# Performance work log

Hardware: AMD Instinct MI355X
Metric: run time of the kernel (lower is better)

Reference implementation:

```python
import jax, jax.numpy as jnp
import numpy as np

N, B, NPG, E = 16384, 64, 256, 524288
F_IN, POS_DIM, L_PE = 32, 3, 8
W, HEADS, LAYERS, DFF = 256, 8, 2, 1024
HID, OUT = 512, 64
S = NPG + 1
DH = W // HEADS


def _ln(x, s, b, eps=1e-5):
    m = jnp.mean(x, -1, keepdims=True)
    v = jnp.var(x, -1, keepdims=True)
    return (x - m) * jax.lax.rsqrt(v + eps) * s + b


def _gelu(x):
    # custom tanh-approx GELU from the source module
    c = float(np.sqrt(2.0 / np.pi))
    return 0.5 * x * (1.0 + jnp.tanh(c * (x + 0.044715 * x ** 3)))


def setup_inputs() -> dict:
    key = jax.random.key(0)
    ks = jax.random.split(key, 24)
    nrm = lambda k, shape, s=0.05: jax.random.normal(k, shape, jnp.float32) * s
    D_IN = F_IN + POS_DIM * L_PE  # 56
    inp = {}
    inp['x'] = jax.random.normal(ks[0], (N, F_IN), jnp.float32)
    inp['p'] = jax.random.uniform(ks[1], (N, POS_DIM), jnp.float32, -1.0, 1.0)
    inp['edge_index'] = jax.random.randint(ks[2], (2, E), 0, N, jnp.int32)
    inp['batch'] = (jnp.arange(N) // NPG).astype(jnp.int32)  # sorted, 64 equal graphs
    inp['gcn_w'] = nrm(ks[3], (D_IN, W), 0.1)
    inp['gcn_b'] = jnp.zeros((W,), jnp.float32)
    inp['cls_token'] = nrm(ks[4], (1, 1, W), 0.02)
    inp['ln_pre_s'] = jnp.ones((W,), jnp.float32)
    inp['ln_pre_b'] = jnp.zeros((W,), jnp.float32)
    inp['norm1_s'] = jnp.ones((LAYERS, W), jnp.float32)
    inp['norm1_b'] = jnp.zeros((LAYERS, W), jnp.float32)
    inp['in_proj_w'] = nrm(ks[5], (LAYERS, W, 3 * W))
    inp['in_proj_b'] = jnp.zeros((LAYERS, 3 * W), jnp.float32)
    inp['out_proj_w'] = nrm(ks[6], (LAYERS, W, W))
    inp['out_proj_b'] = jnp.zeros((LAYERS, W), jnp.float32)
    inp['norm2_s'] = jnp.ones((LAYERS, W), jnp.float32)
    inp['norm2_b'] = jnp.zeros((LAYERS, W), jnp.float32)
    inp['ff_w1'] = nrm(ks[7], (LAYERS, W, DFF))
    inp['ff_b1'] = jnp.zeros((LAYERS, DFF), jnp.float32)
    inp['ff_w2'] = nrm(ks[8], (LAYERS, DFF, W))
    inp['ff_b2'] = jnp.zeros((LAYERS, W), jnp.float32)
    inp['ln_post_s'] = jnp.ones((W,), jnp.float32)
    inp['ln_post_b'] = jnp.zeros((W,), jnp.float32)
    inp['dec_w1'] = nrm(ks[9], (W, HID))
    inp['dec_b1'] = jnp.zeros((HID,), jnp.float32)
    inp['dec_w2'] = nrm(ks[10], (HID, HID))
    inp['dec_b2'] = jnp.zeros((HID,), jnp.float32)
    inp['dec_w3'] = nrm(ks[11], (HID, OUT))
    inp['dec_b3'] = jnp.zeros((OUT,), jnp.float32)
    return inp


def _forward(x, p, gcn_w, gcn_b, cls_token, ln_pre_s, ln_pre_b, norm1_s, norm1_b,
             in_proj_w, in_proj_b, out_proj_w, out_proj_b, norm2_s, norm2_b,
             ff_w1, ff_b1, ff_w2, ff_b2, ln_post_s, ln_post_b,
             dec_w1, dec_b1, dec_w2, dec_b2, dec_w3, dec_b3, edge_index, batch):
    # positional encoding: sin(p * 2^i * pi), i = 0..L-1
    freqs = (2.0 ** jnp.arange(L_PE, dtype=jnp.float32)) * jnp.pi
    pe = jnp.sin(p[:, :, None] * freqs).reshape(N, POS_DIM * L_PE)
    xc = jnp.concatenate([x, pe], axis=-1)  # [N, 56]
    # GCNConv: x W, then sym-normalized aggregation with self loops, + bias
    xw = xc @ gcn_w  # [N, W]
    loop = jnp.arange(N, dtype=edge_index.dtype)
    row = jnp.concatenate([edge_index[0], loop])
    col = jnp.concatenate([edge_index[1], loop])
    deg = jax.ops.segment_sum(jnp.ones_like(row, dtype=xw.dtype), col, num_segments=N)
    dinv = jax.lax.rsqrt(jnp.maximum(deg, 1e-12))
    coef = dinv[row] * dinv[col]
    h = jax.ops.segment_sum(coef[:, None] * xw[row], col, num_segments=N) + gcn_b
    # to_dense_batch (batch is sorted graph ids)
    counts = jax.ops.segment_sum(jnp.ones((N,), jnp.int32), batch, num_segments=B)
    ptr = jnp.concatenate([jnp.zeros((1,), jnp.int32), jnp.cumsum(counts)[:-1]])
    pos = jnp.arange(N, dtype=jnp.int32) - ptr[batch]
    dense = jnp.zeros((B, NPG, W), h.dtype).at[batch, pos].set(h)
    mask = jnp.zeros((B, NPG), bool).at[batch, pos].set(True)
    # prepend cls token
    xd = jnp.concatenate([jnp.broadcast_to(cls_token, (B, 1, W)), dense], axis=1)  # [B,S,W]
    valid = jnp.concatenate([jnp.ones((B, 1), bool), mask], axis=1)  # [B,S]
    xd = _ln(xd, ln_pre_s, ln_pre_b)
    # causal mask with row 0 (cls) unmasked
    am = jnp.triu(jnp.ones((S, S), bool), k=1)
    am = am.at[0, :].set(False)
    allowed = (~am)[None, :, :] & valid[:, None, :]  # [B,S,S]
    scale = 1.0 / float(np.sqrt(DH))
    for l in range(LAYERS):
        h1 = _ln(xd, norm1_s[l], norm1_b[l])
        qkv = h1 @ in_proj_w[l] + in_proj_b[l]  # [B,S,3W]
        q, k, v = jnp.split(qkv, 3, axis=-1)
        q = q.reshape(B, S, HEADS, DH)
        k = k.reshape(B, S, HEADS, DH)
        v = v.reshape(B, S, HEADS, DH)
        sc = jnp.einsum('bqhd,bkhd->bhqk', q, k) * scale
        sc = jnp.where(allowed[:, None, :, :], sc, -1e9)
        a = jax.nn.softmax(sc, axis=-1)
        o = jnp.einsum('bhqk,bkhd->bqhd', a, v).reshape(B, S, W)
        xd = xd + (o @ out_proj_w[l] + out_proj_b[l])
        h2 = _ln(xd, norm2_s[l], norm2_b[l])
        # MLP(num_layers=2) applies activation after BOTH layers (incl. last)
        ff = _gelu(_gelu(h2 @ ff_w1[l] + ff_b1[l]) @ ff_w2[l] + ff_b2[l])
        xd = xd + ff
    cls = _ln(xd[:, 0, :], ln_post_s, ln_post_b)
    # decoder MLP(num_layers=3) with relu after every layer (incl. last)
    h3 = jax.nn.relu(cls @ dec_w1 + dec_b1)
    h3 = jax.nn.relu(h3 @ dec_w2 + dec_b2)
    return jax.nn.relu(h3 @ dec_w3 + dec_b3)


def reference(x, p, gcn_w, gcn_b, cls_token, ln_pre_s, ln_pre_b, norm1_s, norm1_b,
              in_proj_w, in_proj_b, out_proj_w, out_proj_b, norm2_s, norm2_b,
              ff_w1, ff_b1, ff_w2, ff_b2, ln_post_s, ln_post_b,
              dec_w1, dec_b1, dec_w2, dec_b2, dec_w3, dec_b3, edge_index, batch):
    return _forward(x, p, gcn_w, gcn_b, cls_token, ln_pre_s, ln_pre_b, norm1_s, norm1_b,
                    in_proj_w, in_proj_b, out_proj_w, out_proj_b, norm2_s, norm2_b,
                    ff_w1, ff_b1, ff_w2, ff_b2, ln_post_s, ln_post_b,
                    dec_w1, dec_b1, dec_w2, dec_b2, dec_w3, dec_b3, edge_index, batch)
```

## Files before the change

kernel.cpp:

```cpp
#include <hip/hip_runtime.h>
#include <math.h>

constexpr int N_NODES = 16384;
constexpr int BGRAPH  = 64;
constexpr int NEDGE   = 524288;
constexpr int SEQ     = 257;
constexpr int WDIM    = 256;
constexpr int DFF     = 1024;
constexpr int HID     = 512;
constexpr int MROWS   = BGRAPH * SEQ;

constexpr size_t F_Y    = 0;
constexpr size_t F_AGG  = F_Y    + (size_t)N_NODES * 64;
constexpr size_t F_XD   = F_AGG  + (size_t)N_NODES * 64;
constexpr size_t F_CLS  = F_XD   + (size_t)MROWS * WDIM;
constexpr size_t F_D1   = F_CLS  + (size_t)BGRAPH * WDIM;
constexpr size_t F_D2   = F_D1   + (size_t)BGRAPH * HID;
constexpr size_t F_WPAD = F_D2   + (size_t)BGRAPH * HID;
constexpr size_t F_DINV = F_WPAD + (size_t)64 * WDIM;
constexpr size_t F_IEND = F_DINV + (size_t)N_NODES;

typedef __attribute__((ext_vector_type(8))) __bf16 bf16x8;
typedef __attribute__((ext_vector_type(4))) __bf16 bf16x4;
typedef __attribute__((ext_vector_type(4))) float f32x4;

__device__ __forceinline__ float gelu_f(float x) {
    float u = 0.7978845608028654f * (x + 0.044715f * x * x * x);
    return 0.5f * x * (1.0f + tanhf(u));
}

__global__ __launch_bounds__(256) void hist_kernel(const int* __restrict__ col, int* __restrict__ indeg) {
    int e = blockIdx.x * 256 + threadIdx.x;
    atomicAdd(&indeg[col[e]], 1);
}

__global__ __launch_bounds__(1024) void scan_kernel(const int* __restrict__ indeg, int* __restrict__ offs,
                                                    int* __restrict__ cursor, float* __restrict__ dinv) {
    __shared__ int parts[1024];
    int t = threadIdx.x;
    int base = t * 16;
    int loc[16];
    int s = 0;
#pragma unroll
    for (int i = 0; i < 16; ++i) { loc[i] = indeg[base + i]; s += loc[i]; }
    parts[t] = s;
    __syncthreads();
    for (int off = 1; off < 1024; off <<= 1) {
        int v = (t >= off) ? parts[t - off] : 0;
        __syncthreads();
        parts[t] += v;
        __syncthreads();
    }
    int run = (t == 0) ? 0 : parts[t - 1];
#pragma unroll
    for (int i = 0; i < 16; ++i) {
        offs[base + i] = run;
        cursor[base + i] = run;
        dinv[base + i] = rsqrtf((float)loc[i] + 1.0f);
        run += loc[i];
    }
    if (t == 1023) offs[N_NODES] = run;
}

__global__ __launch_bounds__(256) void fill_kernel(const int* __restrict__ ei, int* __restrict__ cursor,
                                                   int* __restrict__ csr) {
    int e = blockIdx.x * 256 + threadIdx.x;
    int r = ei[e];
    int c = ei[NEDGE + e];
    int pos = atomicAdd(&cursor[c], 1);
    csr[pos] = r;
}

__global__ __launch_bounds__(256) void y_kernel(const float* __restrict__ x, const float* __restrict__ p,
                                                const float* __restrict__ dinv, float* __restrict__ y) {
    int idx = blockIdx.x * 256 + threadIdx.x;
    int i = idx >> 6, d = idx & 63;
    float v = 0.f;
    if (d < 32) {
        v = x[i * 32 + d];
    } else if (d < 56) {
        int dd = d - 32;
        int dim = dd >> 3, j = dd & 7;
        v = sinf(p[i * 3 + dim] * (3.14159265358979323846f * (float)(1 << j)));
    }
    y[idx] = dinv[i] * v;
}

__global__ __launch_bounds__(256) void agg_kernel(const float* __restrict__ y, const float* __restrict__ dinv,
                                                  const int* __restrict__ offs, const int* __restrict__ csr,
                                                  float* __restrict__ agg) {
    int c = (blockIdx.x * 256 + threadIdx.x) >> 6;
    int lane = threadIdx.x & 63;
    float acc = y[(size_t)c * 64 + lane];
    int s = offs[c], e = offs[c + 1];
    for (int j = s; j < e; ++j) {
        int r = csr[j];
        acc += y[(size_t)r * 64 + lane];
    }
    agg[(size_t)c * 64 + lane] = dinv[c] * acc;
}

__global__ __launch_bounds__(256) void wpad_kernel(const float* __restrict__ w, float* __restrict__ wp) {
    int idx = blockIdx.x * 256 + threadIdx.x;
    wp[idx] = (idx < 56 * 256) ? w[idx] : 0.f;
}

__global__ __launch_bounds__(256) void cls_write(const float* __restrict__ tok, float* __restrict__ xd) {
    xd[(size_t)blockIdx.x * SEQ * WDIM + threadIdx.x] = tok[threadIdx.x];
}

template <int OUTBF>
__global__ __launch_bounds__(256) void ln4_kernel(const float* __restrict__ in, int rin_stride,
                                                  void* __restrict__ out,
                                                  const float* __restrict__ g, const float* __restrict__ be) {
    int w = threadIdx.x >> 6, lane = threadIdx.x & 63;
    int row = blockIdx.x * 4 + w;
    const float* ip = in + (size_t)row * rin_stride + lane * 4;
    f32x4 v = *(const f32x4*)ip;
    float s = v[0] + v[1] + v[2] + v[3];
    float ss = v[0] * v[0] + v[1] * v[1] + v[2] * v[2] + v[3] * v[3];
#pragma unroll
    for (int off = 1; off < 64; off <<= 1) { s += __shfl_xor(s, off); ss += __shfl_xor(ss, off); }
    float mean = s * 0.00390625f;
    float var = ss * 0.00390625f - mean * mean;
    float rs = rsqrtf(var + 1e-5f);
    f32x4 gv = *(const f32x4*)(g + lane * 4);
    f32x4 bv = *(const f32x4*)(be + lane * 4);
    if (OUTBF) {
        bf16x4 o;
#pragma unroll
        for (int i = 0; i < 4; ++i) o[i] = (__bf16)((v[i] - mean) * rs * gv[i] + bv[i]);
        *(bf16x4*)((__bf16*)out + (size_t)row * 256 + lane * 4) = o;
    } else {
        f32x4 o;
#pragma unroll
        for (int i = 0; i < 4; ++i) o[i] = (v[i] - mean) * rs * gv[i] + bv[i];
        *(f32x4*)((float*)out + (size_t)row * 256 + lane * 4) = o;
    }
}

__global__ __launch_bounds__(256) void tcast_kernel(const float* __restrict__ W, __bf16* __restrict__ Wt,
                                                    int K, int N) {
    __shared__ __bf16 T[64][65];
    int t = threadIdx.x;
    int k0 = blockIdx.x << 6, n0 = blockIdx.y << 6;
#pragma unroll
    for (int i = 0; i < 16; ++i) {
        int idx = t + i * 256;
        int k = idx >> 6, n = idx & 63;
        T[k][n] = (__bf16)W[(size_t)(k0 + k) * N + n0 + n];
    }
    __syncthreads();
#pragma unroll
    for (int i = 0; i < 16; ++i) {
        int idx = t + i * 256;
        int n = idx >> 6, k = idx & 63;
        Wt[(size_t)(n0 + n) * K + k0 + k] = T[k][n];
    }
}

constexpr int LP = 36;
template <int BN, int ACT, int OMODE>
__global__ __launch_bounds__(256) void gemm_bf(const __bf16* __restrict__ A, int lda,
                                               const __bf16* __restrict__ Bt,
                                               const float* __restrict__ bias,
                                               void* __restrict__ Cv, int ldc,
                                               int Ktot, int Mrows, int MBlocks, int NY) {
    constexpr int NTW = BN / 32;
    constexpr int AH = 128 * LP;
    constexpr int BH = BN * LP;
    __shared__ __bf16 As[2 * 128 * LP];
    __shared__ __bf16 Bs[2 * BN * LP];
    int f = blockIdx.x;
    int m8 = f & 7;
    int rest = f >> 3;
    int mg = rest / NY;
    int yb = rest - mg * NY;
    int mb = mg * 8 + m8;
    if (mb >= MBlocks) return;
    int m0 = mb << 7, n0 = yb * BN;

    int t = threadIdx.x;
    int w = t >> 6, L = t & 63;
    int wm = w >> 1, wn = w & 1;
    int lc = L & 15, quad = L >> 4;

    int sa_row = t >> 1, sa_off = (t & 1) << 4;
    const __bf16* ap = A + (size_t)(m0 + sa_row) * lda + sa_off;
    __bf16* as_dst = &As[sa_row * LP + sa_off];
    const __bf16* bp;
    __bf16* bs_dst;
    if constexpr (BN == 128) {
        bp = Bt + (size_t)(n0 + sa_row) * Ktot + sa_off;
        bs_dst = &Bs[sa_row * LP + sa_off];
    } else {
        int sb_row = t >> 2, sb_off = (t & 3) << 3;
        bp = Bt + (size_t)(n0 + sb_row) * Ktot + sb_off;
        bs_dst = &Bs[sb_row * LP + sb_off];
    }

    int a_base = (wm * 64 + lc) * LP + quad * 8;
    int b_base = (wn * (BN / 2) + lc) * LP + quad * 8;

    f32x4 acc[4][NTW] = {};

    bf16x8 ea0, ea1, eb0, eb1, oa0, oa1, ob0, ob1;
    ea0 = *(const bf16x8*)(ap);        ea1 = *(const bf16x8*)(ap + 8);
    oa0 = *(const bf16x8*)(ap + 32);   oa1 = *(const bf16x8*)(ap + 40);
    if constexpr (BN == 128) {
        eb0 = *(const bf16x8*)(bp);        eb1 = *(const bf16x8*)(bp + 8);
        ob0 = *(const bf16x8*)(bp + 32);   ob1 = *(const bf16x8*)(bp + 40);
    } else {
        eb0 = *(const bf16x8*)(bp);
        ob0 = *(const bf16x8*)(bp + 32);
    }

    for (int k0 = 0; k0 < Ktot; k0 += 64) {
        __syncthreads();
        *(bf16x8*)as_dst = ea0;
        *(bf16x8*)(as_dst + 8) = ea1;
        *(bf16x8*)(as_dst + AH) = oa0;
        *(bf16x8*)(as_dst + AH + 8) = oa1;
        if constexpr (BN == 128) {
            *(bf16x8*)bs_dst = eb0;
            *(bf16x8*)(bs_dst + 8) = eb1;
            *(bf16x8*)(bs_dst + BH) = ob0;
            *(bf16x8*)(bs_dst + BH + 8) = ob1;
        } else {
            *(bf16x8*)bs_dst = eb0;
            *(bf16x8*)(bs_dst + BH) = ob0;
        }
        __syncthreads();
        if (k0 + 64 < Ktot) {
            ea0 = *(const bf16x8*)(ap + k0 + 64);
            ea1 = *(const bf16x8*)(ap + k0 + 72);
            oa0 = *(const bf16x8*)(ap + k0 + 96);
            oa1 = *(const bf16x8*)(ap + k0 + 104);
            if constexpr (BN == 128) {
                eb0 = *(const bf16x8*)(bp + k0 + 64);
                eb1 = *(const bf16x8*)(bp + k0 + 72);
                ob0 = *(const bf16x8*)(bp + k0 + 96);
                ob1 = *(const bf16x8*)(bp + k0 + 104);
            } else {
                eb0 = *(const bf16x8*)(bp + k0 + 64);
                ob0 = *(const bf16x8*)(bp + k0 + 96);
            }
        }
        {
            bf16x8 af[4], bfr[NTW];
#pragma unroll
            for (int i = 0; i < 4; ++i) af[i] = *(const bf16x8*)&As[a_base + i * 16 * LP];
#pragma unroll
            for (int i = 0; i < NTW; ++i) bfr[i] = *(const bf16x8*)&Bs[b_base + i * 16 * LP];
#pragma unroll
            for (int mt = 0; mt < 4; ++mt)
#pragma unroll
                for (int nt = 0; nt < NTW; ++nt)
                    acc[mt][nt] = __builtin_amdgcn_mfma_f32_16x16x32_bf16(af[mt], bfr[nt], acc[mt][nt], 0, 0, 0);
        }
        {
            bf16x8 af[4], bfr[NTW];
#pragma unroll
            for (int i = 0; i < 4; ++i) af[i] = *(const bf16x8*)&As[AH + a_base + i * 16 * LP];
#pragma unroll
            for (int i = 0; i < NTW; ++i) bfr[i] = *(const bf16x8*)&Bs[BH + b_base + i * 16 * LP];
#pragma unroll
            for (int mt = 0; mt < 4; ++mt)
#pragma unroll
                for (int nt = 0; nt < NTW; ++nt)
                    acc[mt][nt] = __builtin_amdgcn_mfma_f32_16x16x32_bf16(af[mt], bfr[nt], acc[mt][nt], 0, 0, 0);
        }
    }

#pragma unroll
    for (int mt = 0; mt < 4; ++mt) {
        int gmb = m0 + wm * 64 + mt * 16 + quad * 4;
#pragma unroll
        for (int nt = 0; nt < NTW; ++nt) {
            int gn = n0 + wn * (BN / 2) + nt * 16 + lc;
            float bv = bias[gn];
#pragma unroll
            for (int r = 0; r < 4; ++r) {
                int gm = gmb + r;
                if (gm >= Mrows) continue;
                float v = acc[mt][nt][r] + bv;
                if (ACT == 1) v = gelu_f(v);
                if (OMODE == 0) {
                    ((__bf16*)Cv)[(size_t)gm * ldc + gn] = (__bf16)v;
                } else {
                    float* cp = (float*)Cv + (size_t)gm * ldc + gn;
                    *cp = v + *cp;
                }
            }
        }
    }
}

constexpr int PPITCH = 284;
__global__ __launch_bounds__(256, 2) void attn_mfma(const __bf16* __restrict__ qkvb,
                                                    __bf16* __restrict__ obuf) {
    __shared__ __bf16 Vt[32][PPITCH];
    __shared__ __bf16 Pb[4][16][PPITCH];
    int bb = blockIdx.x;
    int b = bb >> 3, h = bb & 7;
    int t = threadIdx.x;
    int w = t >> 6, L = t & 63;
    int c = L & 15, quad = L >> 4;
    const float scale = 0.17677669529663687f;
    const __bf16* qb = qkvb + (size_t)(b * SEQ) * 768 + h * 32;
    const __bf16* kb = qb + 256;
    const __bf16* vb = qb + 512;
    __bf16* ob = obuf + (size_t)(b * SEQ) * 256 + h * 32;

    for (int idx = t; idx < 272 * 4; idx += 256) {
        int key = idx >> 2, dc = (idx & 3) * 8;
        bf16x8 vv = {};
        if (key < SEQ) vv = *(const bf16x8*)(vb + (size_t)key * 768 + dc);
#pragma unroll
        for (int j = 0; j < 8; ++j) Vt[dc + j][key] = vv[j];
    }

    bf16x8 kfr[17];
#pragma unroll
    for (int tt = 0; tt < 17; ++tt) {
        int kr = tt * 16 + c; if (kr > 256) kr = 256;
        kfr[tt] = *(const bf16x8*)(kb + (size_t)kr * 768 + quad * 8);
    }
    __syncthreads();

#pragma unroll 1
    for (int qt = 0; qt < 5; ++qt) {
        int q0 = qt * 64 + w * 16;
        if (q0 > 256) continue;
        int ntiles = (qt == 0 && w == 0) ? 17 : (qt * 4 + w + 1);
        if (ntiles > 17) ntiles = 17;
        int nkc = (ntiles + 1) >> 1;

        bf16x8 qf;
        {
            int qr = q0 + c; if (qr > 256) qr = 256;
            qf = *(const bf16x8*)(qb + (size_t)qr * 768 + quad * 8);
        }

        f32x4 acc[17];
#pragma unroll
        for (int tt = 0; tt < 17; ++tt) {
            if (tt >= ntiles) continue;
            f32x4 z = {0.f, 0.f, 0.f, 0.f};
            acc[tt] = __builtin_amdgcn_mfma_f32_16x16x32_bf16(qf, kfr[tt], z, 0, 0, 0);
        }

        float inv[4];
#pragma unroll
        for (int j = 0; j < 4; ++j) {
            int q = q0 + quad * 4 + j;
            float mx = -3.0e38f;
#pragma unroll
            for (int tt = 0; tt < 17; ++tt) {
                if (tt >= ntiles) continue;
                int key = tt * 16 + c;
                bool ok = (key < SEQ) && (q == 0 || key <= q);
                float v = ok ? acc[tt][j] * scale : -3.0e38f;
                mx = fmaxf(mx, v);
            }
            mx = fmaxf(mx, __shfl_xor(mx, 1));
            mx = fmaxf(mx, __shfl_xor(mx, 2));
            mx = fmaxf(mx, __shfl_xor(mx, 4));
            mx = fmaxf(mx, __shfl_xor(mx, 8));
            float s = 0.f;
#pragma unroll
            for (int tt = 0; tt < 17; ++tt) {
                if (tt >= ntiles) continue;
                int key = tt * 16 + c;
                bool ok = (key < SEQ) && (q == 0 || key <= q);
                float pv = ok ? expf(acc[tt][j] * scale - mx) : 0.f;
                s += pv;
                Pb[w][quad * 4 + j][key] = (__bf16)pv;
            }
            if ((ntiles & 1) && ntiles < 17)
                Pb[w][quad * 4 + j][ntiles * 16 + c] = (__bf16)0.f;
            s += __shfl_xor(s, 1);
            s += __shfl_xor(s, 2);
            s += __shfl_xor(s, 4);
            s += __shfl_xor(s, 8);
            inv[j] = 1.0f / s;
        }

        f32x4 oacc0 = {0.f, 0.f, 0.f, 0.f};
        f32x4 oacc1 = {0.f, 0.f, 0.f, 0.f};
#pragma unroll
        for (int kc = 0; kc < 9; ++kc) {
            if (kc >= nkc) continue;
            int off = kc * 32 + quad * 8;
            bf16x8 af = {};
            bf16x8 bf0 = {};
            bf16x8 bf1 = {};
            if (off < 257) {
                af  = *(const bf16x8*)&Pb[w][c][off];
                bf0 = *(const bf16x8*)&Vt[c][off];
                bf1 = *(const bf16x8*)&Vt[16 + c][off];
            }
            oacc0 = __builtin_amdgcn_mfma_f32_16x16x32_bf16(af, bf0, oacc0, 0, 0, 0);
            oacc1 = __builtin_amdgcn_mfma_f32_16x16x32_bf16(af, bf1, oacc1, 0, 0, 0);
        }

#pragma unroll
        for (int j = 0; j < 4; ++j) {
            int q = q0 + quad * 4 + j;
            if (q < SEQ) {
                __bf16* op = ob + (size_t)q * 256;
                op[c]      = (__bf16)(oacc0[j] * inv[j]);
                op[16 + c] = (__bf16)(oacc1[j] * inv[j]);
            }
        }
    }
}

template <int ACT, bool RESID, bool REMAP>
__global__ __launch_bounds__(256) void gemm_std(const float* __restrict__ A, int lda,
                                                const float* __restrict__ Bw, int ldb,
                                                const float* __restrict__ bias,
                                                float* __restrict__ C, int ldc, int Ktot) {
    int t = threadIdx.x;
    int m0 = blockIdx.x << 6, n0 = blockIdx.y << 6;
    __shared__ float As[16][68];
    __shared__ float Bs[16][64];
    int arow = t >> 2, akk = (t & 3) << 2;
    int bk = t >> 4, bn = (t & 15) << 2;
    int tm = (t >> 4) << 2, tn = (t & 15) << 2;
    float acc[4][4] = {};
    const float* ap = A + (size_t)(m0 + arow) * lda + akk;
    const float* bp = Bw + (size_t)bk * ldb + n0 + bn;
    for (int k0 = 0; k0 < Ktot; k0 += 16) {
        float4 av = *(const float4*)(ap + k0);
        float4 bv = *(const float4*)(bp + (size_t)k0 * ldb);
        __syncthreads();
        As[akk + 0][arow] = av.x; As[akk + 1][arow] = av.y;
        As[akk + 2][arow] = av.z; As[akk + 3][arow] = av.w;
        *(float4*)&Bs[bk][bn] = bv;
        __syncthreads();
#pragma unroll
        for (int k = 0; k < 16; ++k) {
            float4 a = *(const float4*)&As[k][tm];
            float4 b = *(const float4*)&Bs[k][tn];
            acc[0][0] += a.x * b.x; acc[0][1] += a.x * b.y; acc[0][2] += a.x * b.z; acc[0][3] += a.x * b.w;
            acc[1][0] += a.y * b.x; acc[1][1] += a.y * b.y; acc[1][2] += a.y * b.z; acc[1][3] += a.y * b.w;
            acc[2][0] += a.z * b.x; acc[2][1] += a.z * b.y; acc[2][2] += a.z * b.z; acc[2][3] += a.z * b.w;
            acc[3][0] += a.w * b.x; acc[3][1] += a.w * b.y; acc[3][2] += a.w * b.z; acc[3][3] += a.w * b.w;
        }
    }
#pragma unroll
    for (int i = 0; i < 4; ++i) {
        int gm = m0 + tm + i;
        int orow = REMAP ? (gm + (gm >> 8) + 1) : gm;
        float* cp = C + (size_t)orow * ldc + n0 + tn;
        float4 r;
        r.x = acc[i][0] + bias[n0 + tn + 0];
        r.y = acc[i][1] + bias[n0 + tn + 1];
        r.z = acc[i][2] + bias[n0 + tn + 2];
        r.w = acc[i][3] + bias[n0 + tn + 3];
        if (ACT == 1) { r.x = gelu_f(r.x); r.y = gelu_f(r.y); r.z = gelu_f(r.z); r.w = gelu_f(r.w); }
        if (ACT == 2) { r.x = fmaxf(r.x, 0.f); r.y = fmaxf(r.y, 0.f); r.z = fmaxf(r.z, 0.f); r.w = fmaxf(r.w, 0.f); }
        if (RESID) {
            float4 o = *(const float4*)cp;
            r.x += o.x; r.y += o.y; r.z += o.z; r.w += o.w;
        }
        *(float4*)cp = r;
    }
}

template <int K, int NOUT>
__global__ __launch_bounds__(256) void dec_fc2(const float* __restrict__ in, const float* __restrict__ w,
                                               const float* __restrict__ bia, float* __restrict__ out) {
    __shared__ float rowbuf[K];
    __shared__ float part[4][64];
    int b = blockIdx.x, c = blockIdx.y, t = threadIdx.x;
    for (int i = t; i < K; i += 256) rowbuf[i] = in[(size_t)b * K + i];
    __syncthreads();
    int lane = t & 63, wv = t >> 6;
    int n = c * 64 + lane;
    const int KQ = K / 4;
    const float* wp = w + (size_t)(wv * KQ) * NOUT + n;
    float s = 0.f;
#pragma unroll 8
    for (int k = 0; k < KQ; ++k) s += rowbuf[wv * KQ + k] * wp[(size_t)k * NOUT];
    part[wv][lane] = s;
    __syncthreads();
    if (wv == 0) {
        float r = part[0][lane] + part[1][lane] + part[2][lane] + part[3][lane] + bia[n];
        out[(size_t)b * NOUT + n] = fmaxf(r, 0.f);
    }
}

extern "C" void kernel_launch(void* const* d_in, const int* in_sizes, int n_in,
                              void* d_out, int out_size, void* d_ws, size_t ws_size,
                              hipStream_t stream) {
    const float* x         = (const float*)d_in[0];
    const float* p         = (const float*)d_in[1];
    const int*   ei        = (const int*)d_in[2];
    const float* gcn_w     = (const float*)d_in[4];
    const float* gcn_b     = (const float*)d_in[5];
    const float* cls_tok   = (const float*)d_in[6];
    const float* ln_pre_s  = (const float*)d_in[7];
    const float* ln_pre_b  = (const float*)d_in[8];
    const float* norm1_s   = (const float*)d_in[9];
    const float* norm1_b   = (const float*)d_in[10];
    const float* in_proj_w = (const float*)d_in[11];
    const float* in_proj_b = (const float*)d_in[12];
    const float* out_proj_w= (const float*)d_in[13];
    const float* out_proj_b= (const float*)d_in[14];
    const float* norm2_s   = (const float*)d_in[15];
    const float* norm2_b   = (const float*)d_in[16];
    const float* ff_w1     = (const float*)d_in[17];
    const float* ff_b1     = (const float*)d_in[18];
    const float* ff_w2     = (const float*)d_in[19];
    const float* ff_b2     = (const float*)d_in[20];
    const float* ln_post_s = (const float*)d_in[21];
    const float* ln_post_b = (const float*)d_in[22];
    const float* dec_w1    = (const float*)d_in[23];
    const float* dec_b1    = (const float*)d_in[24];
    const float* dec_w2    = (const float*)d_in[25];
    const float* dec_b2    = (const float*)d_in[26];
    const float* dec_w3    = (const float*)d_in[27];
    const float* dec_b3    = (const float*)d_in[28];

    float* ws   = (float*)d_ws;
    float* y    = ws + F_Y;
    float* agg  = ws + F_AGG;
    float* xd   = ws + F_XD;
    float* cls  = ws + F_CLS;
    float* dd1  = ws + F_D1;
    float* dd2  = ws + F_D2;
    float* wpad = ws + F_WPAD;
    float* dinv = ws + F_DINV;
    int* ibase  = (int*)(ws + F_IEND);
    int* indeg  = ibase;
    int* offs   = ibase + N_NODES;
    int* cursor = offs + N_NODES + 1;
    int* csr    = cursor + N_NODES;
    uintptr_t ub = ((uintptr_t)(csr + NEDGE) + 15) & ~(uintptr_t)15;
    __bf16* h1b  = (__bf16*)ub;
    __bf16* qkvb = h1b  + (size_t)MROWS * 256;
    __bf16* ffbb = qkvb + (size_t)MROWS * 768;
    __bf16* wt_in  = ffbb  + (size_t)MROWS * 1024;
    __bf16* wt_out = wt_in  + 2 * 768 * 256;
    __bf16* wt_f1  = wt_out + 2 * 256 * 256;
    __bf16* wt_f2  = wt_f1  + 2 * 1024 * 256;

    hipMemsetAsync(indeg, 0, N_NODES * sizeof(int), stream);
    hist_kernel<<<NEDGE / 256, 256, 0, stream>>>(ei + NEDGE, indeg);
    scan_kernel<<<1, 1024, 0, stream>>>(indeg, offs, cursor, dinv);
    fill_kernel<<<NEDGE / 256, 256, 0, stream>>>(ei, cursor, csr);
    y_kernel<<<N_NODES * 64 / 256, 256, 0, stream>>>(x, p, dinv, y);
    agg_kernel<<<N_NODES / 4, 256, 0, stream>>>(y, dinv, offs, csr, agg);
    wpad_kernel<<<64, 256, 0, stream>>>(gcn_w, wpad);

    for (int l = 0; l < 2; ++l) {
        tcast_kernel<<<dim3(4, 12), 256, 0, stream>>>(in_proj_w + (size_t)l * 256 * 768,
                                                      wt_in + (size_t)l * 768 * 256, 256, 768);
        tcast_kernel<<<dim3(4, 4), 256, 0, stream>>>(out_proj_w + (size_t)l * 256 * 256,
                                                     wt_out + (size_t)l * 256 * 256, 256, 256);
        tcast_kernel<<<dim3(4, 16), 256, 0, stream>>>(ff_w1 + (size_t)l * 256 * 1024,
                                                      wt_f1 + (size_t)l * 1024 * 256, 256, 1024);
        tcast_kernel<<<dim3(16, 4), 256, 0, stream>>>(ff_w2 + (size_t)l * 1024 * 256,
                                                      wt_f2 + (size_t)l * 256 * 1024, 1024, 256);
    }

    gemm_std<0, false, true><<<dim3(256, 4), 256, 0, stream>>>(agg, 64, wpad, 256, gcn_b, xd, 256, 64);
    cls_write<<<64, 256, 0, stream>>>(cls_tok, xd);
    ln4_kernel<0><<<MROWS / 4, 256, 0, stream>>>(xd, 256, xd, ln_pre_s, ln_pre_b);

    const int MB = (MROWS + 127) / 128;
    const int MG8 = (MB + 7) / 8;
    for (int l = 0; l < 2; ++l) {
        ln4_kernel<1><<<MROWS / 4, 256, 0, stream>>>(xd, 256, h1b, norm1_s + l * WDIM, norm1_b + l * WDIM);
        gemm_bf<128, 0, 0><<<8 * 6 * MG8, 256, 0, stream>>>(
            h1b, 256, wt_in + (size_t)l * 768 * 256, in_proj_b + l * 768, qkvb, 768, 256, MROWS, MB, 6);
        attn_mfma<<<512, 256, 0, stream>>>(qkvb, h1b);
        gemm_bf<64, 0, 1><<<8 * 4 * MG8, 256, 0, stream>>>(
            h1b, 256, wt_out + (size_t)l * 256 * 256, out_proj_b + l * WDIM, xd, 256, 256, MROWS, MB, 4);
        ln4_kernel<1><<<MROWS / 4, 256, 0, stream>>>(xd, 256, h1b, norm2_s + l * WDIM, norm2_b + l * WDIM);
        gemm_bf<128, 1, 0><<<8 * 8 * MG8, 256, 0, stream>>>(
            h1b, 256, wt_f1 + (size_t)l * 1024 * 256, ff_b1 + l * DFF, ffbb, 1024, 256, MROWS, MB, 8);
        gemm_bf<64, 1, 1><<<8 * 4 * MG8, 256, 0, stream>>>(
            ffbb, 1024, wt_f2 + (size_t)l * 256 * 1024, ff_b2 + l * WDIM, xd, 256, 1024, MROWS, MB, 4);
    }

    ln4_kernel<0><<<BGRAPH / 4, 256, 0, stream>>>(xd, SEQ * WDIM, cls, ln_post_s, ln_post_b);
    dec_fc2<256, 512><<<dim3(BGRAPH, 8), 256, 0, stream>>>(cls, dec_w1, dec_b1, dd1);
    dec_fc2<512, 512><<<dim3(BGRAPH, 8), 256, 0, stream>>>(dd1, dec_w2, dec_b2, dd2);
    dec_fc2<512, 64><<<dim3(BGRAPH, 1), 256, 0, stream>>>(dd2, dec_w3, dec_b3, (float*)d_out);
}
```

Before: 714.4 us.

## Compute only the CLS row in the last transformer layer

Only the CLS token of the final layer feeds the output, so the last layer now computes K and V projections for all rows and runs everything else on the CLS row alone. That covers the Q projection, attention, out-projection, LN2 and the FFN, each done in small dedicated kernels over 64 rows. This removes most of the last layer's GEMM and attention work and skips transposing the unused layer-2 weights. The new per-row kernels are simple scalar fp32 loops and may be slow relative to their tiny work, and they mix fp32 and bf16 precision differently than the main path.

```diff
diff --git a/kernel.cpp b/kernel.cpp
--- a/kernel.cpp
+++ b/kernel.cpp
@@ -18,7 +18,8 @@
 constexpr size_t F_D2   = F_D1   + (size_t)BGRAPH * HID;
 constexpr size_t F_WPAD = F_D2   + (size_t)BGRAPH * HID;
 constexpr size_t F_DINV = F_WPAD + (size_t)64 * WDIM;
-constexpr size_t F_IEND = F_DINV + (size_t)N_NODES;
+constexpr size_t F_XCLS = F_DINV + (size_t)N_NODES;
+constexpr size_t F_IEND = F_XCLS + (size_t)BGRAPH * WDIM;
 
 typedef __attribute__((ext_vector_type(8))) __bf16 bf16x8;
 typedef __attribute__((ext_vector_type(4))) __bf16 bf16x4;
@@ -414,6 +415,127 @@
             }
         }
     }
+}
+
+__global__ __launch_bounds__(256) void qcls_kernel(const __bf16* __restrict__ h1b,
+                                                   const float* __restrict__ W,
+                                                   const float* __restrict__ bias,
+                                                   __bf16* __restrict__ qcls) {
+    __shared__ float hrow[256];
+    int b = blockIdx.x, t = threadIdx.x;
+    hrow[t] = (float)h1b[(size_t)(b * SEQ) * 256 + t];
+    __syncthreads();
+    float s = bias[t];
+    for (int k = 0; k < 256; ++k) s += hrow[k] * W[(size_t)k * 768 + t];
+    qcls[b * 256 + t] = (__bf16)s;
+}
+
+__global__ __launch_bounds__(64) void attn_cls(const __bf16* __restrict__ qcls,
+                                               const __bf16* __restrict__ qkvb,
+                                               __bf16* __restrict__ ocls) {
+    __shared__ float p[260];
+    int bb = blockIdx.x;
+    int b = bb >> 3, h = bb & 7;
+    int lane = threadIdx.x;
+    const float scale = 0.17677669529663687f;
+    float q[32];
+    const __bf16* qp = qcls + b * 256 + h * 32;
+#pragma unroll
+    for (int c = 0; c < 4; ++c) {
+        bf16x8 v = *(const bf16x8*)(qp + c * 8);
+#pragma unroll
+        for (int e = 0; e < 8; ++e) q[c * 8 + e] = (float)v[e];
+    }
+    float sc[5];
+    float mx = -3.0e38f;
+#pragma unroll
+    for (int i = 0; i < 5; ++i) {
+        int j = lane + i * 64;
+        float s = -3.0e38f;
+        if (j < SEQ) {
+            const __bf16* kp = qkvb + (size_t)(b * SEQ + j) * 768 + 256 + h * 32;
+            float a = 0.f;
+#pragma unroll
+            for (int c = 0; c < 4; ++c) {
+                bf16x8 v = *(const bf16x8*)(kp + c * 8);
+#pragma unroll
+                for (int e = 0; e < 8; ++e) a += q[c * 8 + e] * (float)v[e];
+            }
+            s = a * scale;
+        }
+        sc[i] = s;
+        mx = fmaxf(mx, s);
+    }
+#pragma unroll
+    for (int off = 1; off < 64; off <<= 1) mx = fmaxf(mx, __shfl_xor(mx, off));
+    float sum = 0.f;
+#pragma unroll
+    for (int i = 0; i < 5; ++i) {
+        int j = lane + i * 64;
+        float e = (j < SEQ) ? expf(sc[i] - mx) : 0.f;
+        sc[i] = e;
+        sum += e;
+    }
+#pragma unroll
+    for (int off = 1; off < 64; off <<= 1) sum += __shfl_xor(sum, off);
+    float inv = 1.0f / sum;
+#pragma unroll
+    for (int i = 0; i < 5; ++i) {
+        int j = lane + i * 64;
+        if (j < SEQ) p[j] = sc[i] * inv;
+    }
+    __syncthreads();
+    if (lane < 32) {
+        float o = 0.f;
+        for (int j = 0; j < SEQ; ++j)
+            o += p[j] * (float)qkvb[(size_t)(b * SEQ + j) * 768 + 512 + h * 32 + lane];
+        ocls[b * 256 + h * 32 + lane] = (__bf16)o;
+    }
+}
+
+__global__ __launch_bounds__(256) void oproj_cls(const __bf16* __restrict__ ocls,
+                                                 const float* __restrict__ W,
+                                                 const float* __restrict__ bias,
+                                                 const float* __restrict__ xd,
+                                                 float* __restrict__ xcls) {
+    __shared__ float orow[256];
+    int b = blockIdx.x, t = threadIdx.x;
+    orow[t] = (float)ocls[b * 256 + t];
+    __syncthreads();
+    float s = bias[t];
+    for (int k = 0; k < 256; ++k) s += orow[k] * W[(size_t)k * 256 + t];
+    xcls[b * 256 + t] = s + xd[(size_t)(b * SEQ) * 256 + t];
+}
+
+__global__ __launch_bounds__(256) void ff1_cls(const __bf16* __restrict__ h2cls,
+                                               const float* __restrict__ W1,
+                                               const float* __restrict__ b1,
+                                               __bf16* __restrict__ f1cls) {
+    __shared__ float hrow[256];
+    int b = blockIdx.x, t = threadIdx.x;
+    hrow[t] = (float)h2cls[b * 256 + t];
+    __syncthreads();
+#pragma unroll
+    for (int i = 0; i < 4; ++i) {
+        int col = t + i * 256;
+        float s = b1[col];
+        for (int k = 0; k < 256; ++k) s += hrow[k] * W1[(size_t)k * 1024 + col];
+        f1cls[b * 1024 + col] = (__bf16)gelu_f(s);
+    }
+}
+
+__global__ __launch_bounds__(256) void ff2_cls(const __bf16* __restrict__ f1cls,
+                                               const float* __restrict__ W2,
+                                               const float* __restrict__ b2,
+                                               float* __restrict__ xcls) {
+    __shared__ float frow[1024];
+    int b = blockIdx.x, t = threadIdx.x;
+#pragma unroll
+    for (int i = 0; i < 4; ++i) frow[t + i * 256] = (float)f1cls[b * 1024 + t + i * 256];
+    __syncthreads();
+    float s = b2[t];
+    for (int k = 0; k < 1024; ++k) s += frow[k] * W2[(size_t)k * 256 + t];
+    xcls[b * 256 + t] += gelu_f(s);
 }
 
 template <int ACT, bool RESID, bool REMAP>
@@ -533,6 +655,7 @@
     float* dd2  = ws + F_D2;
     float* wpad = ws + F_WPAD;
     float* dinv = ws + F_DINV;
+    float* xcls = ws + F_XCLS;
     int* ibase  = (int*)(ws + F_IEND);
     int* indeg  = ibase;
     int* offs   = ibase + N_NODES;
@@ -546,6 +669,10 @@
     __bf16* wt_out = wt_in  + 2 * 768 * 256;
     __bf16* wt_f1  = wt_out + 2 * 256 * 256;
     __bf16* wt_f2  = wt_f1  + 2 * 1024 * 256;
+    __bf16* qcls   = wt_f2 + 2 * 256 * 1024;
+    __bf16* ocls   = qcls + 64 * 256;
+    __bf16* h2cls  = ocls + 64 * 256;
+    __bf16* f1cls  = h2cls + 64 * 256;
 
     hipMemsetAsync(indeg, 0, N_NODES * sizeof(int), stream);
     hist_kernel<<<NEDGE / 256, 256, 0, stream>>>(ei + NEDGE, indeg);
@@ -555,16 +682,12 @@
     agg_kernel<<<N_NODES / 4, 256, 0, stream>>>(y, dinv, offs, csr, agg);
     wpad_kernel<<<64, 256, 0, stream>>>(gcn_w, wpad);
 
-    for (int l = 0; l < 2; ++l) {
-        tcast_kernel<<<dim3(4, 12), 256, 0, stream>>>(in_proj_w + (size_t)l * 256 * 768,
-                                                      wt_in + (size_t)l * 768 * 256, 256, 768);
-        tcast_kernel<<<dim3(4, 4), 256, 0, stream>>>(out_proj_w + (size_t)l * 256 * 256,
-                                                     wt_out + (size_t)l * 256 * 256, 256, 256);
-        tcast_kernel<<<dim3(4, 16), 256, 0, stream>>>(ff_w1 + (size_t)l * 256 * 1024,
-                                                      wt_f1 + (size_t)l * 1024 * 256, 256, 1024);
-        tcast_kernel<<<dim3(16, 4), 256, 0, stream>>>(ff_w2 + (size_t)l * 1024 * 256,
-                                                      wt_f2 + (size_t)l * 256 * 1024, 1024, 256);
-    }
+    tcast_kernel<<<dim3(4, 12), 256, 0, stream>>>(in_proj_w, wt_in, 256, 768);
+    tcast_kernel<<<dim3(4, 4), 256, 0, stream>>>(out_proj_w, wt_out, 256, 256);
+    tcast_kernel<<<dim3(4, 16), 256, 0, stream>>>(ff_w1, wt_f1, 256, 1024);
+    tcast_kernel<<<dim3(16, 4), 256, 0, stream>>>(ff_w2, wt_f2, 1024, 256);
+    tcast_kernel<<<dim3(4, 12), 256, 0, stream>>>(in_proj_w + (size_t)256 * 768,
+                                                  wt_in + (size_t)768 * 256, 256, 768);
 
     gemm_std<0, false, true><<<dim3(256, 4), 256, 0, stream>>>(agg, 64, wpad, 256, gcn_b, xd, 256, 64);
     cls_write<<<64, 256, 0, stream>>>(cls_tok, xd);
@@ -572,21 +695,31 @@
 
     const int MB = (MROWS + 127) / 128;
     const int MG8 = (MB + 7) / 8;
-    for (int l = 0; l < 2; ++l) {
-        ln4_kernel<1><<<MROWS / 4, 256, 0, stream>>>(xd, 256, h1b, norm1_s + l * WDIM, norm1_b + l * WDIM);
-        gemm_bf<128, 0, 0><<<8 * 6 * MG8, 256, 0, stream>>>(
-            h1b, 256, wt_in + (size_t)l * 768 * 256, in_proj_b + l * 768, qkvb, 768, 256, MROWS, MB, 6);
-        attn_mfma<<<512, 256, 0, stream>>>(qkvb, h1b);
-        gemm_bf<64, 0, 1><<<8 * 4 * MG8, 256, 0, stream>>>(
-            h1b, 256, wt_out + (size_t)l * 256 * 256, out_proj_b + l * WDIM, xd, 256, 256, MROWS, MB, 4);
-        ln4_kernel<1><<<MROWS / 4, 256, 0, stream>>>(xd, 256, h1b, norm2_s + l * WDIM, norm2_b + l * WDIM);
-        gemm_bf<128, 1, 0><<<8 * 8 * MG8, 256, 0, stream>>>(
-            h1b, 256, wt_f1 + (size_t)l * 1024 * 256, ff_b1 + l * DFF, ffbb, 1024, 256, MROWS, MB, 8);
-        gemm_bf<64, 1, 1><<<8 * 4 * MG8, 256, 0, stream>>>(
-            ffbb, 1024, wt_f2 + (size_t)l * 256 * 1024, ff_b2 + l * WDIM, xd, 256, 1024, MROWS, MB, 4);
-    }
-
-    ln4_kernel<0><<<BGRAPH / 4, 256, 0, stream>>>(xd, SEQ * WDIM, cls, ln_post_s, ln_post_b);
+
+    ln4_kernel<1><<<MROWS / 4, 256, 0, stream>>>(xd, 256, h1b, norm1_s, norm1_b);
+    gemm_bf<128, 0, 0><<<8 * 6 * MG8, 256, 0, stream>>>(
+        h1b, 256, wt_in, in_proj_b, qkvb, 768, 256, MROWS, MB, 6);
+    attn_mfma<<<512, 256, 0, stream>>>(qkvb, h1b);
+    gemm_bf<64, 0, 1><<<8 * 4 * MG8, 256, 0, stream>>>(
+        h1b, 256, wt_out, out_proj_b, xd, 256, 256, MROWS, MB, 4);
+    ln4_kernel<1><<<MROWS / 4, 256, 0, stream>>>(xd, 256, h1b, norm2_s, norm2_b);
+    gemm_bf<128, 1, 0><<<8 * 8 * MG8, 256, 0, stream>>>(
+        h1b, 256, wt_f1, ff_b1, ffbb, 1024, 256, MROWS, MB, 8);
+    gemm_bf<64, 1, 1><<<8 * 4 * MG8, 256, 0, stream>>>(
+        ffbb, 1024, wt_f2, ff_b2, xd, 256, 1024, MROWS, MB, 4);
+
+    ln4_kernel<1><<<MROWS / 4, 256, 0, stream>>>(xd, 256, h1b, norm1_s + WDIM, norm1_b + WDIM);
+    gemm_bf<128, 0, 0><<<8 * 4 * MG8, 256, 0, stream>>>(
+        h1b, 256, wt_in + (size_t)768 * 256 + (size_t)256 * 256,
+        in_proj_b + 768 + 256, qkvb + 256, 768, 256, MROWS, MB, 4);
+    qcls_kernel<<<64, 256, 0, stream>>>(h1b, in_proj_w + (size_t)256 * 768, in_proj_b + 768, qcls);
+    attn_cls<<<512, 64, 0, stream>>>(qcls, qkvb, ocls);
+    oproj_cls<<<64, 256, 0, stream>>>(ocls, out_proj_w + (size_t)256 * 256, out_proj_b + 256, xd, xcls);
+    ln4_kernel<1><<<16, 256, 0, stream>>>(xcls, 256, h2cls, norm2_s + WDIM, norm2_b + WDIM);
+    ff1_cls<<<64, 256, 0, stream>>>(h2cls, ff_w1 + (size_t)256 * 1024, ff_b1 + 1024, f1cls);
+    ff2_cls<<<64, 256, 0, stream>>>(f1cls, ff_w2 + (size_t)1024 * 256, ff_b2 + 256, xcls);
+
+    ln4_kernel<0><<<16, 256, 0, stream>>>(xcls, 256, cls, ln_post_s, ln_post_b);
     dec_fc2<256, 512><<<dim3(BGRAPH, 8), 256, 0, stream>>>(cls, dec_w1, dec_b1, dd1);
     dec_fc2<512, 512><<<dim3(BGRAPH, 8), 256, 0, stream>>>(dd1, dec_w2, dec_b2, dd2);
     dec_fc2<512, 64><<<dim3(BGRAPH, 1), 256, 0, stream>>>(dd2, dec_w3, dec_b3, (float*)d_out);
```

Measured after the change: 635.0 us. 1.13x faster.
